# Kernel optimization log

Hardware: AMD Instinct MI355X
Metric: run time of the kernel (lower is better)

## Reference

```python
import jax, jax.numpy as jnp
import numpy as np
from jax import lax

KERNEL_SIZES = (3, 5, 7)
EPS = 1e-12  # torch F.normalize default eps


def _gamma(x, k):
    """SpatialCorrelationSampler(kernel_size=k)(x, F.normalize(x, dim=1)).

    With patch_size=1, stride=1, padding=0, dilation=1 the sampler output at
    (b, y, x) is sum over channels and the kxk window of in1 * in2. Since
    in2 = in1 / max(||in1||_c, eps), the channel contraction collapses to
    ||x||^2 / max(||x||, eps) per pixel, followed by a kxk box-sum (VALID).
    x: [B, C, H, W] -> gamma: [B, H-k+1, W-k+1]
    """
    norm = jnp.sqrt(jnp.sum(x * x, axis=1))          # [B, H, W]
    p = (norm * norm) / jnp.maximum(norm, EPS)       # [B, H, W]
    return lax.reduce_window(p, 0.0, lax.add, (1, k, k), (1, 1, 1), 'VALID')


def reference(out_feat0, out_feat1, gt_feat0, gt_feat1):
    loss = jnp.float32(0.0)
    for xo, xg in ((out_feat0, gt_feat0), (out_feat1, gt_feat1)):
        for k in KERNEL_SIZES:
            go = _gamma(xo, k)
            gg = _gamma(xg, k)
            loss = loss + jnp.mean((go - gg) ** 2)   # nn.MSELoss (mean)
    return loss


def setup_inputs() -> dict:
    key = jax.random.key(0)
    k0, k1, k2, k3 = jax.random.split(key, 4)
    return {
        'out_feat0': jax.random.normal(k0, (8, 256, 64, 64), dtype=jnp.float32),
        'out_feat1': jax.random.normal(k1, (8, 512, 32, 32), dtype=jnp.float32),
        'gt_feat0': jax.random.normal(k2, (8, 256, 64, 64), dtype=jnp.float32),
        'gt_feat1': jax.random.normal(k3, (8, 512, 32, 32), dtype=jnp.float32),
    }
```

## Files before the change

kernel.cpp:

```cpp
#include <hip/hip_runtime.h>
#include <math.h>

#define EPS 1e-12f

typedef float f4 __attribute__((ext_vector_type(4)));

template <int PLANE, int C, int CS_N>
__device__ __forceinline__ void partial_tile(
    const float* __restrict__ xo, const float* __restrict__ xg,
    float* __restrict__ part,
    int b, int tile, int cs, int tid, float* lds )
{
    constexpr int SLABF = 256;
    constexpr int CG    = 8;
    constexpr int CPT   = (C / CS_N) / CG;
    static_assert(CPT == 8, "geometry");

    const int quad = tid & 63;
    const int cg   = tid >> 6;
    const int base = b * C * PLANE + tile * SLABF + quad * 4;
    const int c0   = cs * (C / CS_N) + cg * CPT;

    f4 so = {0.f, 0.f, 0.f, 0.f};
    f4 sg = {0.f, 0.f, 0.f, 0.f};
#pragma unroll
    for (int ib = 0; ib < CPT / 4; ++ib) {
        f4 vo[4], vg[4];
#pragma unroll
        for (int u = 0; u < 4; ++u) {
            const int off = base + (c0 + ib * 4 + u) * PLANE;
            vo[u] = __builtin_nontemporal_load(reinterpret_cast<const f4*>(xo + off));
            vg[u] = __builtin_nontemporal_load(reinterpret_cast<const f4*>(xg + off));
        }
#pragma unroll
        for (int u = 0; u < 4; ++u) {
            so += vo[u] * vo[u];
            sg += vg[u] * vg[u];
        }
    }

    *reinterpret_cast<f4*>(lds + (0 * CG + cg) * SLABF + quad * 4) = so;
    *reinterpret_cast<f4*>(lds + (1 * CG + cg) * SLABF + quad * 4) = sg;
    __syncthreads();

    if (tid < 128) {
        const int s = tid >> 6;
        const int q = tid & 63;
        f4 a = {0.f, 0.f, 0.f, 0.f};
#pragma unroll
        for (int g = 0; g < CG; ++g)
            a += *reinterpret_cast<const f4*>(lds + (s * CG + g) * SLABF + q * 4);
        *reinterpret_cast<f4*>(
            part + ((s * 8 + b) * CS_N + cs) * PLANE + tile * SLABF + q * 4) = a;
    }
}

__global__ __launch_bounds__(512) void stage1a_kernel(
    const float* __restrict__ o0, const float* __restrict__ g0,
    const float* __restrict__ o1, const float* __restrict__ g1,
    float* __restrict__ part0, float* __restrict__ part1,
    float* __restrict__ out)
{
    __shared__ float lds[4096];
    const int bid = blockIdx.x;
    if (bid == 0 && threadIdx.x == 0) out[0] = 0.0f;
    if (bid < 512) {
        const int b = bid >> 6, tile = (bid >> 2) & 15, cs = bid & 3;
        partial_tile<4096, 256, 4>(o0, g0, part0, b, tile, cs, threadIdx.x, lds);
    } else {
        const int e = bid - 512;
        const int b = e >> 5, tile = (e >> 3) & 3, cs = e & 7;
        partial_tile<1024, 512, 8>(o1, g1, part1, b, tile, cs, threadIdx.x, lds);
    }
}

__global__ __launch_bounds__(256) void stage2_kernel(
    const float* __restrict__ part0, const float* __restrict__ part1,
    float* __restrict__ out)
{
    __shared__ float d[4096];
    __shared__ float rbuf[64 * 62];
    __shared__ float wsum[4];

    const int bid = blockIdx.x;
    const int t   = bid / 24;
    const int rem = bid % 24;
    const int b   = rem / 3;
    const int ki  = rem % 3;
    const int k   = 3 + 2 * ki;
    const int H   = t ? 32 : 64;
    const int V   = H - k + 1;
    const int PLANE = H * H;
    const int CS  = t ? 8 : 4;
    const float* pb = t ? part1 : part0;
    const int tid = threadIdx.x;

    const float* po = pb + (0 * 8 + b) * CS * PLANE;
    const float* pg = pb + (1 * 8 + b) * CS * PLANE;

    for (int q = tid; q < PLANE / 4; q += 256) {
        f4 ao = {0.f, 0.f, 0.f, 0.f};
        f4 ag = {0.f, 0.f, 0.f, 0.f};
        for (int c = 0; c < CS; ++c) {
            ao += *reinterpret_cast<const f4*>(po + c * PLANE + q * 4);
            ag += *reinterpret_cast<const f4*>(pg + c * PLANE + q * 4);
        }
        f4 dd;
#pragma unroll
        for (int j = 0; j < 4; ++j) {
            const float no = sqrtf(ao[j]);
            const float ng = sqrtf(ag[j]);
            dd[j] = ao[j] / fmaxf(no, EPS) - ag[j] / fmaxf(ng, EPS);
        }
        *reinterpret_cast<f4*>(d + q * 4) = dd;
    }
    __syncthreads();

    for (int i = tid; i < H * V; i += 256) {
        const int y = i / V;
        const int x = i - y * V;
        float s = 0.f;
        for (int j = 0; j < k; ++j) s += d[y * H + x + j];
        rbuf[i] = s;
    }
    __syncthreads();

    float acc = 0.f;
    for (int i = tid; i < V * V; i += 256) {
        const int y = i / V;
        const int x = i - y * V;
        float s = 0.f;
        for (int j = 0; j < k; ++j) s += rbuf[(y + j) * V + x];
        acc = fmaf(s, s, acc);
    }

    for (int off = 32; off > 0; off >>= 1) acc += __shfl_down(acc, off);
    if ((tid & 63) == 0) wsum[tid >> 6] = acc;
    __syncthreads();
    if (tid == 0) {
        const float total = wsum[0] + wsum[1] + wsum[2] + wsum[3];
        atomicAdd(out, total / (float)(8 * V * V));
    }
}

extern "C" void kernel_launch(void* const* d_in, const int* in_sizes, int n_in,
                              void* d_out, int out_size, void* d_ws, size_t ws_size,
                              hipStream_t stream) {
    const float* out_feat0 = (const float*)d_in[0];
    const float* out_feat1 = (const float*)d_in[1];
    const float* gt_feat0  = (const float*)d_in[2];
    const float* gt_feat1  = (const float*)d_in[3];
    float* out = (float*)d_out;

    float* part0 = (float*)d_ws;
    float* part1 = part0 + 2 * 8 * 4 * 4096;

    stage1a_kernel<<<768, 512, 0, stream>>>(
        out_feat0, gt_feat0, out_feat1, gt_feat1, part0, part1, out);
    stage2_kernel<<<48, 256, 0, stream>>>(part0, part1, out);
}
```

Measured before the change: 138.3 us.

## Specialize stage2 on compile-time sizes, double its block size, drop nontemporal loads

The stage2 tail is templated on H, K and CS so the window loops and partial-sum loop unroll with constant trip counts and the integer division by V becomes a constant. Stage2 now runs 512 threads per block instead of 256 to spread the small per-block work over more waves. Separately, the stage1 input loads switch from nontemporal to normal loads, which changes the cache policy on the large streaming read. Each specialization adds code size, and the load-policy change can help or hurt the bandwidth-bound first stage.

After: 122.4 us (median of 2 runs). 11.5% less time.

```diff
diff --git a/kernel.cpp b/kernel.cpp
--- a/kernel.cpp
+++ b/kernel.cpp
@@ -29,8 +29,8 @@
 #pragma unroll
         for (int u = 0; u < 4; ++u) {
             const int off = base + (c0 + ib * 4 + u) * PLANE;
-            vo[u] = __builtin_nontemporal_load(reinterpret_cast<const f4*>(xo + off));
-            vg[u] = __builtin_nontemporal_load(reinterpret_cast<const f4*>(xg + off));
+            vo[u] = *reinterpret_cast<const f4*>(xo + off);
+            vg[u] = *reinterpret_cast<const f4*>(xg + off);
         }
 #pragma unroll
         for (int u = 0; u < 4; ++u) {
@@ -74,33 +74,19 @@
     }
 }
 
-__global__ __launch_bounds__(256) void stage2_kernel(
-    const float* __restrict__ part0, const float* __restrict__ part1,
-    float* __restrict__ out)
+template <int H, int K, int CS>
+__device__ __forceinline__ void tile_mse(
+    const float* __restrict__ po, const float* __restrict__ pg,
+    float* __restrict__ out, int tid,
+    float* d , float* rbuf , float* wsum )
 {
-    __shared__ float d[4096];
-    __shared__ float rbuf[64 * 62];
-    __shared__ float wsum[4];
+    constexpr int V = H - K + 1;
+    constexpr int PLANE = H * H;
 
-    const int bid = blockIdx.x;
-    const int t   = bid / 24;
-    const int rem = bid % 24;
-    const int b   = rem / 3;
-    const int ki  = rem % 3;
-    const int k   = 3 + 2 * ki;
-    const int H   = t ? 32 : 64;
-    const int V   = H - k + 1;
-    const int PLANE = H * H;
-    const int CS  = t ? 8 : 4;
-    const float* pb = t ? part1 : part0;
-    const int tid = threadIdx.x;
-
-    const float* po = pb + (0 * 8 + b) * CS * PLANE;
-    const float* pg = pb + (1 * 8 + b) * CS * PLANE;
-
-    for (int q = tid; q < PLANE / 4; q += 256) {
+    for (int q = tid; q < PLANE / 4; q += 512) {
         f4 ao = {0.f, 0.f, 0.f, 0.f};
         f4 ag = {0.f, 0.f, 0.f, 0.f};
+#pragma unroll
         for (int c = 0; c < CS; ++c) {
             ao += *reinterpret_cast<const f4*>(po + c * PLANE + q * 4);
             ag += *reinterpret_cast<const f4*>(pg + c * PLANE + q * 4);
@@ -116,21 +102,23 @@
     }
     __syncthreads();
 
-    for (int i = tid; i < H * V; i += 256) {
+    for (int i = tid; i < H * V; i += 512) {
         const int y = i / V;
         const int x = i - y * V;
         float s = 0.f;
-        for (int j = 0; j < k; ++j) s += d[y * H + x + j];
+#pragma unroll
+        for (int j = 0; j < K; ++j) s += d[y * H + x + j];
         rbuf[i] = s;
     }
     __syncthreads();
 
     float acc = 0.f;
-    for (int i = tid; i < V * V; i += 256) {
+    for (int i = tid; i < V * V; i += 512) {
         const int y = i / V;
         const int x = i - y * V;
         float s = 0.f;
-        for (int j = 0; j < k; ++j) s += rbuf[(y + j) * V + x];
+#pragma unroll
+        for (int j = 0; j < K; ++j) s += rbuf[(y + j) * V + x];
         acc = fmaf(s, s, acc);
     }
 
@@ -138,8 +126,40 @@
     if ((tid & 63) == 0) wsum[tid >> 6] = acc;
     __syncthreads();
     if (tid == 0) {
-        const float total = wsum[0] + wsum[1] + wsum[2] + wsum[3];
+        float total = 0.f;
+#pragma unroll
+        for (int wv = 0; wv < 8; ++wv) total += wsum[wv];
         atomicAdd(out, total / (float)(8 * V * V));
+    }
+}
+
+__global__ __launch_bounds__(512) void stage2_kernel(
+    const float* __restrict__ part0, const float* __restrict__ part1,
+    float* __restrict__ out)
+{
+    __shared__ float d[4096];
+    __shared__ float rbuf[64 * 62];
+    __shared__ float wsum[8];
+
+    const int bid = blockIdx.x;
+    const int t   = bid / 24;
+    const int rem = bid % 24;
+    const int b   = rem / 3;
+    const int ki  = rem % 3;
+    const int tid = threadIdx.x;
+
+    if (t == 0) {
+        const float* po = part0 + (0 * 8 + b) * 4 * 4096;
+        const float* pg = part0 + (1 * 8 + b) * 4 * 4096;
+        if      (ki == 0) tile_mse<64, 3, 4>(po, pg, out, tid, d, rbuf, wsum);
+        else if (ki == 1) tile_mse<64, 5, 4>(po, pg, out, tid, d, rbuf, wsum);
+        else              tile_mse<64, 7, 4>(po, pg, out, tid, d, rbuf, wsum);
+    } else {
+        const float* po = part1 + (0 * 8 + b) * 8 * 1024;
+        const float* pg = part1 + (1 * 8 + b) * 8 * 1024;
+        if      (ki == 0) tile_mse<32, 3, 8>(po, pg, out, tid, d, rbuf, wsum);
+        else if (ki == 1) tile_mse<32, 5, 8>(po, pg, out, tid, d, rbuf, wsum);
+        else              tile_mse<32, 7, 8>(po, pg, out, tid, d, rbuf, wsum);
     }
 }
 
@@ -157,5 +177,5 @@
 
     stage1a_kernel<<<768, 512, 0, stream>>>(
         out_feat0, gt_feat0, out_feat1, gt_feat1, part0, part1, out);
-    stage2_kernel<<<48, 256, 0, stream>>>(part0, part1, out);
+    stage2_kernel<<<48, 512, 0, stream>>>(part0, part1, out);
 }
```
